# Kernel optimization log

Measured on AMD Instinct MI355X. Metric: run time of the kernel, lower is better.

The kernel has to match this reference:

```python
import jax, jax.numpy as jnp
import numpy as np

N_EMBD = 768
N_HEAD = 12
HEAD_DIM = N_EMBD // N_HEAD


def setup_inputs() -> dict:
    key = jax.random.key(0)
    k0, k1, k2, k3, k4 = jax.random.split(key, 5)
    B, T, C = 2, 4096, N_EMBD
    x = jax.random.normal(k0, (B, T, C), dtype=jnp.float32)
    # c_attn: Linear(C, 3C); c_proj: Linear(C, C). torch Linear: y = x @ W.T + b
    s = 1.0 / np.sqrt(C)
    W_attn = jax.random.uniform(k1, (3 * C, C), dtype=jnp.float32, minval=-s, maxval=s)
    b_attn = jax.random.uniform(k2, (3 * C,), dtype=jnp.float32, minval=-s, maxval=s)
    W_proj = jax.random.uniform(k3, (C, C), dtype=jnp.float32, minval=-s, maxval=s)
    b_proj = jax.random.uniform(k4, (C,), dtype=jnp.float32, minval=-s, maxval=s)
    return {"x": x, "W_attn": W_attn, "b_attn": b_attn, "W_proj": W_proj, "b_proj": b_proj}


def reference(x, W_attn, b_attn, W_proj, b_proj):
    B, T, C = x.shape
    H, D = N_HEAD, HEAD_DIM
    qkv = x @ W_attn.T + b_attn                      # [B,T,3C]
    q, k, v = jnp.split(qkv, 3, axis=-1)
    # [B,T,C] -> [B,H,T,D]
    q = q.reshape(B, T, H, D).transpose(0, 2, 1, 3)
    k = k.reshape(B, T, H, D).transpose(0, 2, 1, 3)
    v = v.reshape(B, T, H, D).transpose(0, 2, 1, 3)
    scale = 1.0 / jnp.sqrt(jnp.asarray(D, dtype=x.dtype))
    att = jnp.einsum('bhqd,bhkd->bhqk', q, k) * scale  # [B,H,T,T]
    att = jax.nn.softmax(att, axis=-1)
    y = jnp.einsum('bhqk,bhkd->bhqd', att, v)          # [B,H,T,D]
    y = y.transpose(0, 2, 1, 3).reshape(B, T, C)
    return y @ W_proj.T + b_proj
```

## Files before the change

### kernel.cpp

```cpp
#include <hip/hip_runtime.h>
#include <stdint.h>
#include <stddef.h>

typedef __bf16 bf16_t;
typedef bf16_t bf16x4 __attribute__((ext_vector_type(4)));
typedef bf16_t bf16x8 __attribute__((ext_vector_type(8)));
typedef float  f32x4  __attribute__((ext_vector_type(4)));
typedef _Float16 f16_t;
typedef f16_t f16x4 __attribute__((ext_vector_type(4)));

#define MFMA_BF16_K32(a, b, c) __builtin_amdgcn_mfma_f32_16x16x32_bf16(a, b, c, 0, 0, 0)
#define MFMA_F16_K16(a, b, c)  __builtin_amdgcn_mfma_f32_16x16x16f16(a, b, c, 0, 0, 0)

__device__ __forceinline__ void gload_lds16(const void* g, void* l) {
    __builtin_amdgcn_global_load_lds(
        (const __attribute__((address_space(1))) void*)g,
        (__attribute__((address_space(3))) void*)l,
        16, 0, 0);
}

#define NX 1572864
#define NWA 442368
#define NWP 147456
__global__ void cvt_all(const float* __restrict__ x, const float* __restrict__ Wa,
                        const float* __restrict__ Wp, bf16_t* __restrict__ xb,
                        bf16_t* __restrict__ Wab, bf16_t* __restrict__ Wpb) {
    int i = blockIdx.x * blockDim.x + threadIdx.x;
    const float4* src; bf16_t* dst; int j;
    if (i < NX)            { src = (const float4*)x;  dst = xb;  j = i; }
    else if (i < NX + NWA) { src = (const float4*)Wa; dst = Wab; j = i - NX; }
    else                   { src = (const float4*)Wp; dst = Wpb; j = i - NX - NWA; }
    float4 f = src[j];
    bf16x4 o = { (bf16_t)f.x, (bf16_t)f.y, (bf16_t)f.z, (bf16_t)f.w };
    ((bf16x4*)dst)[j] = o;
}

template <int KDIM>
__device__ __forceinline__ void gemm_mainloop(
    const bf16_t* __restrict__ A, const bf16_t* __restrict__ Bt,
    bf16_t* As, bf16_t* Bs, int m0, int n0, int wave, int lane, f32x4 acc[4][4])
{
    const int quad = lane >> 4, l15 = lane & 15;
    const int wm = ((wave >> 1) << 6), wn = ((wave & 1) << 6);

    const int srow = (wave << 4) + (lane >> 2);
    const int sw   = (((lane & 3) ^ ((srow >> 1) & 3)) << 3);
    const bf16_t* gA = A  + (size_t)(m0 + srow) * KDIM + sw;
    const bf16_t* gB = Bt + (size_t)(n0 + srow) * KDIM + sw;
    bf16_t* lA0 = As + wave * 512;
    bf16_t* lA1 = As + 2048 + wave * 512;
    bf16_t* lB0 = Bs + wave * 512;
    bf16_t* lB1 = Bs + 2048 + wave * 512;

    const int xorv = ((quad ^ ((l15 >> 1) & 3)) << 3);

    for (int k0 = 0; k0 < KDIM; k0 += 32) {
        __syncthreads();
        gload_lds16(gA + k0,                       lA0);
        gload_lds16(gA + (size_t)64 * KDIM + k0,   lA1);
        gload_lds16(gB + k0,                       lB0);
        gload_lds16(gB + (size_t)64 * KDIM + k0,   lB1);
        __syncthreads();

        bf16x8 af[4], bfr[4];
#pragma unroll
        for (int t = 0; t < 4; t++) {
            af[t]  = *(const bf16x8*)(As + (wm + t * 16 + l15) * 32 + xorv);
            bfr[t] = *(const bf16x8*)(Bs + (wn + t * 16 + l15) * 32 + xorv);
        }
#pragma unroll
        for (int mt = 0; mt < 4; mt++)
#pragma unroll
            for (int nt = 0; nt < 4; nt++)
                acc[mt][nt] = MFMA_BF16_K32(af[mt], bfr[nt], acc[mt][nt]);
    }
}

__global__ __launch_bounds__(256) void gemm_qkv(
    const bf16_t* __restrict__ A,
    const bf16_t* __restrict__ Bt,
    const float* __restrict__ bias,
    bf16_t* __restrict__ qo, bf16_t* __restrict__ ko, f16_t* __restrict__ vo)
{
    __shared__ bf16_t As[128 * 32];
    __shared__ bf16_t Bs[128 * 32];
    const int tid = threadIdx.x, wave = tid >> 6, lane = tid & 63;
    const int quad = lane >> 4, l15 = lane & 15;
    const int m0 = blockIdx.y * 128, n0 = blockIdx.x * 128;
    f32x4 acc[4][4] = {};
    gemm_mainloop<768>(A, Bt, As, Bs, m0, n0, wave, lane, acc);

    const int wm = ((wave >> 1) << 6), wn = ((wave & 1) << 6);
#pragma unroll
    for (int nt = 0; nt < 4; nt++) {
        const int cc = n0 + wn + nt * 16 + l15;
        const float bia = bias[cc];
        const int which = cc / 768;
        const int rem = cc - which * 768;
        const int h = rem >> 6, d = rem & 63;
        if (which < 2) {
            bf16_t* dst = (which == 0) ? qo : ko;
#pragma unroll
            for (int mt = 0; mt < 4; mt++) {
#pragma unroll
                for (int r = 0; r < 4; r++) {
                    const int row = m0 + wm + mt * 16 + quad * 4 + r;
                    const int b = row >> 12, t = row & 4095;
                    dst[((size_t)(b * 12 + h) * 4096 + t) * 64 + d] =
                        (bf16_t)(acc[mt][nt][r] + bia);
                }
            }
        } else {
#pragma unroll
            for (int mt = 0; mt < 4; mt++) {
                const int row0 = m0 + wm + mt * 16 + quad * 4;
                const int b = row0 >> 12, t0 = row0 & 4095;
                f16x4 ov = { (f16_t)(acc[mt][nt][0] + bia),
                             (f16_t)(acc[mt][nt][1] + bia),
                             (f16_t)(acc[mt][nt][2] + bia),
                             (f16_t)(acc[mt][nt][3] + bia) };
                *(f16x4*)(vo + ((size_t)(b * 12 + h) * 64 + d) * 4096 + t0) = ov;
            }
        }
    }
}

__global__ __launch_bounds__(256) void gemm_proj(
    const bf16_t* __restrict__ A,
    const bf16_t* __restrict__ Bt,
    const float* __restrict__ bias,
    float* __restrict__ out)
{
    __shared__ bf16_t As[128 * 32];
    __shared__ bf16_t Bs[128 * 32];
    const int tid = threadIdx.x, wave = tid >> 6, lane = tid & 63;
    const int quad = lane >> 4, l15 = lane & 15;
    const int m0 = blockIdx.y * 128, n0 = blockIdx.x * 128;
    f32x4 acc[4][4] = {};
    gemm_mainloop<768>(A, Bt, As, Bs, m0, n0, wave, lane, acc);

    const int wm = ((wave >> 1) << 6), wn = ((wave & 1) << 6);
#pragma unroll
    for (int nt = 0; nt < 4; nt++) {
        const int cc = n0 + wn + nt * 16 + l15;
        const float bia = bias[cc];
#pragma unroll
        for (int mt = 0; mt < 4; mt++) {
#pragma unroll
            for (int r = 0; r < 4; r++) {
                const int row = m0 + wm + mt * 16 + quad * 4 + r;
                out[(size_t)row * 768 + cc] = acc[mt][nt][r] + bia;
            }
        }
    }
}

#define QSCALE 0.1803368801f
__global__ __launch_bounds__(256, 5) void attn_fwd(
    const bf16_t* __restrict__ qg, const bf16_t* __restrict__ kg,
    const f16_t* __restrict__ vtg, bf16_t* __restrict__ y)
{
    __shared__ bf16_t Ks0[64 * 64], Ks1[64 * 64];
    __shared__ f16_t  Vt0[64 * 64], Vt1[64 * 64];
    const int tid = threadIdx.x, wave = tid >> 6, lane = tid & 63;
    const int quad = lane >> 4, l15 = lane & 15;

    const int blk = blockIdx.x;
    const int xcd = blk & 7;
    const int idx = blk >> 3;
    const int hl  = idx % 3;
    const int qt  = idx / 3;
    const int bh  = xcd * 3 + hl;
    const int b = bh / 12, h = bh - b * 12;
    const size_t base = (size_t)bh * 4096 * 64;
    const bf16_t* kgt = kg + base;
    const f16_t*  vgt = vtg + base;

    const int qrow = qt * 64 + wave * 16 + l15;
    bf16x8 qf[2];
    qf[0] = *(const bf16x8*)(qg + base + (size_t)qrow * 64 + quad * 8);
    qf[1] = *(const bf16x8*)(qg + base + (size_t)qrow * 64 + 32 + quad * 8);
#pragma unroll
    for (int j = 0; j < 8; j++) {
        qf[0][j] = (bf16_t)((float)qf[0][j] * QSCALE);
        qf[1][j] = (bf16_t)((float)qf[1][j] * QSCALE);
    }

    f32x4 O[4] = {};
    float psum = 0.f;

    const int srow8 = tid >> 3;
    const int sc8   = (tid & 7) ^ (srow8 & 7);
    const int ksoff = (quad ^ (l15 & 7)) << 3;
    const int l8 = l15 & 7, q1 = quad >> 1, q0off = (quad & 1) * 8;

    auto stage = [&](int kt, bf16_t* Kd, f16_t* Vd) {
        const bf16_t* kp = kgt + (size_t)kt * 64 * 64;
        const f16_t*  vp = vgt + kt * 64;
#pragma unroll
        for (int i = 0; i < 2; i++) {
            gload_lds16(kp + (i * 32 + srow8) * 64 + sc8 * 8,           Kd + (i * 256 + tid) * 8);
            gload_lds16(vp + (size_t)(i * 32 + srow8) * 4096 + sc8 * 8, Vd + (i * 256 + tid) * 8);
        }
    };

    auto compute = [&](const bf16_t* ks, const f16_t* vs) {
        f32x4 sc[4];
#pragma unroll
        for (int ct = 0; ct < 4; ct++) {
            const bf16_t* kr = ks + (ct * 16 + l15) * 64;
            bf16x8 kf0 = *(const bf16x8*)(kr + ksoff);
            bf16x8 kf1 = *(const bf16x8*)(kr + (ksoff ^ 32));
            f32x4 s = {};
            s = MFMA_BF16_K32(kf0, qf[0], s);
            s = MFMA_BF16_K32(kf1, qf[1], s);
            sc[ct] = s;
        }
        f16x4 pf[4];
#pragma unroll
        for (int ct = 0; ct < 4; ct++) {
            float e0 = exp2f(sc[ct][0]), e1 = exp2f(sc[ct][1]);
            float e2 = exp2f(sc[ct][2]), e3 = exp2f(sc[ct][3]);
            psum += (e0 + e1) + (e2 + e3);
            f16x4 p = { (f16_t)e0, (f16_t)e1, (f16_t)e2, (f16_t)e3 };
            pf[ct] = p;
        }
#pragma unroll
        for (int dt = 0; dt < 4; dt++) {
            const char* vr = (const char*)(vs + (dt * 16 + l15) * 64);
#pragma unroll
            for (int kk = 0; kk < 4; kk++) {
                const int slot = ((kk << 1) | q1) ^ l8;
                f16x4 vf = *(const f16x4*)(vr + slot * 16 + q0off);
                O[dt] = MFMA_F16_K16(vf, pf[kk], O[dt]);
            }
        }
    };

    stage(0, Ks0, Vt0);
    for (int kt = 0; kt < 64; kt += 2) {
        __syncthreads();
        stage(kt + 1, Ks1, Vt1);
        compute(Ks0, Vt0);
        __syncthreads();
        if (kt + 2 < 64) stage(kt + 2, Ks0, Vt0);
        compute(Ks1, Vt1);
    }

    psum += __shfl_xor(psum, 16, 64);
    psum += __shfl_xor(psum, 32, 64);
    const float rcp = 1.0f / psum;
    const int t = qt * 64 + wave * 16 + l15;
    bf16_t* yr = y + ((size_t)b * 4096 + t) * 768 + h * 64 + quad * 4;
#pragma unroll
    for (int dt = 0; dt < 4; dt++) {
        bf16x4 ov = { (bf16_t)(O[dt][0] * rcp), (bf16_t)(O[dt][1] * rcp),
                      (bf16_t)(O[dt][2] * rcp), (bf16_t)(O[dt][3] * rcp) };
        *(bf16x4*)(yr + dt * 16) = ov;
    }
}

extern "C" void kernel_launch(void* const* d_in, const int* in_sizes, int n_in,
                              void* d_out, int out_size, void* d_ws, size_t ws_size,
                              hipStream_t stream) {
    const float* x  = (const float*)d_in[0];
    const float* Wa = (const float*)d_in[1];
    const float* ba = (const float*)d_in[2];
    const float* Wp = (const float*)d_in[3];
    const float* bp = (const float*)d_in[4];
    float* out = (float*)d_out;

    char* ws = (char*)d_ws;
    bf16_t* xb  = (bf16_t*)(ws);
    bf16_t* Wab = (bf16_t*)(ws + 12582912);
    bf16_t* Wpb = (bf16_t*)(ws + 16121856);
    bf16_t* qb  = (bf16_t*)(ws + 17301504);
    bf16_t* kb  = (bf16_t*)(ws + 29884416);
    f16_t*  vtb = (f16_t*)(ws + 42467328);
    bf16_t* yb  = (bf16_t*)(ws + 55050240);

    cvt_all<<<8448, 256, 0, stream>>>(x, Wa, Wp, xb, Wab, Wpb);
    gemm_qkv <<<dim3(18, 64), 256, 0, stream>>>(xb, Wab, ba, qb, kb, vtb);
    attn_fwd <<<1536, 256, 0, stream>>>(qb, kb, vtb, yb);
    gemm_proj<<<dim3( 6, 64), 256, 0, stream>>>(yb, Wpb, bp, out);
}
```

Baseline: 329.5 us.

## Split attention keys across waves with LDS reduction of partial outputs

```diff
diff --git a/kernel.cpp b/kernel.cpp
--- a/kernel.cpp
+++ b/kernel.cpp
@@ -156,12 +156,20 @@
 }
 
 #define QSCALE 0.1803368801f
-__global__ __launch_bounds__(256, 5) void attn_fwd(
+__global__ __launch_bounds__(256, 3) void attn_fwd(
     const bf16_t* __restrict__ qg, const bf16_t* __restrict__ kg,
     const f16_t* __restrict__ vtg, bf16_t* __restrict__ y)
 {
-    __shared__ bf16_t Ks0[64 * 64], Ks1[64 * 64];
-    __shared__ f16_t  Vt0[64 * 64], Vt1[64 * 64];
+    __shared__ __align__(16) char smem[36608];
+    bf16_t* Ks0 = (bf16_t*)(smem);
+    bf16_t* Ks1 = (bf16_t*)(smem + 8192);
+    f16_t*  Vt0 = (f16_t*)(smem + 16384);
+    f16_t*  Vt1 = (f16_t*)(smem + 24576);
+    float*  RedA = (float*)(smem);
+    float*  RedB = (float*)(smem + 17408);
+    float*  Psr  = (float*)(smem + 34816);
+    float*  PsT  = (float*)(smem + 35840);
+
     const int tid = threadIdx.x, wave = tid >> 6, lane = tid & 63;
     const int quad = lane >> 4, l15 = lane & 15;
 
@@ -176,23 +184,29 @@
     const bf16_t* kgt = kg + base;
     const f16_t*  vgt = vtg + base;
 
-    const int qrow = qt * 64 + wave * 16 + l15;
-    bf16x8 qf[2];
-    qf[0] = *(const bf16x8*)(qg + base + (size_t)qrow * 64 + quad * 8);
-    qf[1] = *(const bf16x8*)(qg + base + (size_t)qrow * 64 + 32 + quad * 8);
-#pragma unroll
-    for (int j = 0; j < 8; j++) {
-        qf[0][j] = (bf16_t)((float)qf[0][j] * QSCALE);
-        qf[1][j] = (bf16_t)((float)qf[1][j] * QSCALE);
-    }
-
-    f32x4 O[4] = {};
-    float psum = 0.f;
+    bf16x8 qf[4][2];
+#pragma unroll
+    for (int qc = 0; qc < 4; qc++) {
+        const int qrow = qt * 64 + qc * 16 + l15;
+        qf[qc][0] = *(const bf16x8*)(qg + base + (size_t)qrow * 64 + quad * 8);
+        qf[qc][1] = *(const bf16x8*)(qg + base + (size_t)qrow * 64 + 32 + quad * 8);
+#pragma unroll
+        for (int j = 0; j < 8; j++) {
+            qf[qc][0][j] = (bf16_t)((float)qf[qc][0][j] * QSCALE);
+            qf[qc][1][j] = (bf16_t)((float)qf[qc][1][j] * QSCALE);
+        }
+    }
+
+    f32x4 O[4][4] = {};
+    float psum[4] = {};
 
     const int srow8 = tid >> 3;
     const int sc8   = (tid & 7) ^ (srow8 & 7);
-    const int ksoff = (quad ^ (l15 & 7)) << 3;
-    const int l8 = l15 & 7, q1 = quad >> 1, q0off = (quad & 1) * 8;
+    const int l8 = l15 & 7;
+    const int w16 = wave << 4;
+    const int ksoff = (quad ^ l8) << 3;
+    const int vslot = ((wave << 1) | (quad >> 1)) ^ l8;
+    const int q0off = (quad & 1) * 8;
 
     auto stage = [&](int kt, bf16_t* Kd, f16_t* Vd) {
         const bf16_t* kp = kgt + (size_t)kt * 64 * 64;
@@ -205,35 +219,33 @@
     };
 
     auto compute = [&](const bf16_t* ks, const f16_t* vs) {
+        const bf16_t* kr = ks + (w16 + l15) * 64;
+        bf16x8 kf0 = *(const bf16x8*)(kr + ksoff);
+        bf16x8 kf1 = *(const bf16x8*)(kr + (ksoff ^ 32));
         f32x4 sc[4];
 #pragma unroll
-        for (int ct = 0; ct < 4; ct++) {
-            const bf16_t* kr = ks + (ct * 16 + l15) * 64;
-            bf16x8 kf0 = *(const bf16x8*)(kr + ksoff);
-            bf16x8 kf1 = *(const bf16x8*)(kr + (ksoff ^ 32));
+        for (int qc = 0; qc < 4; qc++) {
             f32x4 s = {};
-            s = MFMA_BF16_K32(kf0, qf[0], s);
-            s = MFMA_BF16_K32(kf1, qf[1], s);
-            sc[ct] = s;
+            s = MFMA_BF16_K32(kf0, qf[qc][0], s);
+            s = MFMA_BF16_K32(kf1, qf[qc][1], s);
+            sc[qc] = s;
         }
         f16x4 pf[4];
 #pragma unroll
-        for (int ct = 0; ct < 4; ct++) {
-            float e0 = exp2f(sc[ct][0]), e1 = exp2f(sc[ct][1]);
-            float e2 = exp2f(sc[ct][2]), e3 = exp2f(sc[ct][3]);
-            psum += (e0 + e1) + (e2 + e3);
+        for (int qc = 0; qc < 4; qc++) {
+            float e0 = exp2f(sc[qc][0]), e1 = exp2f(sc[qc][1]);
+            float e2 = exp2f(sc[qc][2]), e3 = exp2f(sc[qc][3]);
+            psum[qc] += (e0 + e1) + (e2 + e3);
             f16x4 p = { (f16_t)e0, (f16_t)e1, (f16_t)e2, (f16_t)e3 };
-            pf[ct] = p;
+            pf[qc] = p;
         }
 #pragma unroll
         for (int dt = 0; dt < 4; dt++) {
             const char* vr = (const char*)(vs + (dt * 16 + l15) * 64);
-#pragma unroll
-            for (int kk = 0; kk < 4; kk++) {
-                const int slot = ((kk << 1) | q1) ^ l8;
-                f16x4 vf = *(const f16x4*)(vr + slot * 16 + q0off);
-                O[dt] = MFMA_F16_K16(vf, pf[kk], O[dt]);
-            }
+            f16x4 vf = *(const f16x4*)(vr + vslot * 16 + q0off);
+#pragma unroll
+            for (int qc = 0; qc < 4; qc++)
+                O[dt][qc] = MFMA_F16_K16(vf, pf[qc], O[dt][qc]);
         }
     };
 
@@ -247,16 +259,69 @@
         compute(Ks1, Vt1);
     }
 
-    psum += __shfl_xor(psum, 16, 64);
-    psum += __shfl_xor(psum, 32, 64);
-    const float rcp = 1.0f / psum;
-    const int t = qt * 64 + wave * 16 + l15;
-    bf16_t* yr = y + ((size_t)b * 4096 + t) * 768 + h * 64 + quad * 4;
-#pragma unroll
-    for (int dt = 0; dt < 4; dt++) {
-        bf16x4 ov = { (bf16_t)(O[dt][0] * rcp), (bf16_t)(O[dt][1] * rcp),
-                      (bf16_t)(O[dt][2] * rcp), (bf16_t)(O[dt][3] * rcp) };
-        *(bf16x4*)(yr + dt * 16) = ov;
+#pragma unroll
+    for (int qc = 0; qc < 4; qc++) {
+        psum[qc] += __shfl_xor(psum[qc], 16, 64);
+        psum[qc] += __shfl_xor(psum[qc], 32, 64);
+    }
+    __syncthreads();
+    if (wave == 2) {
+#pragma unroll
+        for (int dt = 0; dt < 4; dt++)
+#pragma unroll
+            for (int qc = 0; qc < 4; qc++)
+                *(f32x4*)(RedA + (qc * 16 + l15) * 68 + dt * 16 + quad * 4) = O[dt][qc];
+    } else if (wave == 3) {
+#pragma unroll
+        for (int dt = 0; dt < 4; dt++)
+#pragma unroll
+            for (int qc = 0; qc < 4; qc++)
+                *(f32x4*)(RedB + (qc * 16 + l15) * 68 + dt * 16 + quad * 4) = O[dt][qc];
+    }
+    if (quad == 0) {
+#pragma unroll
+        for (int qc = 0; qc < 4; qc++) Psr[wave * 64 + qc * 16 + l15] = psum[qc];
+    }
+    __syncthreads();
+    if (wave == 0) {
+#pragma unroll
+        for (int dt = 0; dt < 4; dt++)
+#pragma unroll
+            for (int qc = 0; qc < 4; qc++)
+                O[dt][qc] += *(const f32x4*)(RedA + (qc * 16 + l15) * 68 + dt * 16 + quad * 4);
+    } else if (wave == 1) {
+#pragma unroll
+        for (int dt = 0; dt < 4; dt++)
+#pragma unroll
+            for (int qc = 0; qc < 4; qc++)
+                O[dt][qc] += *(const f32x4*)(RedB + (qc * 16 + l15) * 68 + dt * 16 + quad * 4);
+    }
+    __syncthreads();
+    if (wave == 1) {
+#pragma unroll
+        for (int dt = 0; dt < 4; dt++)
+#pragma unroll
+            for (int qc = 0; qc < 4; qc++)
+                *(f32x4*)(RedA + (qc * 16 + l15) * 68 + dt * 16 + quad * 4) = O[dt][qc];
+    } else if (wave == 3) {
+        PsT[lane] = Psr[lane] + Psr[64 + lane] + Psr[128 + lane] + Psr[192 + lane];
+    }
+    __syncthreads();
+    if (wave == 0) {
+#pragma unroll
+        for (int qc = 0; qc < 4; qc++) {
+            const float rcp = 1.0f / PsT[qc * 16 + l15];
+            const int t = qt * 64 + qc * 16 + l15;
+            bf16_t* yr = y + ((size_t)b * 4096 + t) * 768 + h * 64 + quad * 4;
+#pragma unroll
+            for (int dt = 0; dt < 4; dt++) {
+                f32x4 o4 = O[dt][qc] +
+                    *(const f32x4*)(RedA + (qc * 16 + l15) * 68 + dt * 16 + quad * 4);
+                bf16x4 ov = { (bf16_t)(o4[0] * rcp), (bf16_t)(o4[1] * rcp),
+                              (bf16_t)(o4[2] * rcp), (bf16_t)(o4[3] * rcp) };
+                *(bf16x4*)(yr + dt * 16) = ov;
+            }
+        }
     }
 }
 
```

Result: faster. 308.8 us (-6.3%).
